# Optimization experiments

Hardware: AMD Instinct MI355X
Metric: run time of the kernel (lower is better)

## Reference

```python
import jax, jax.numpy as jnp
import numpy as np

L, B = 64, 7          # n_layers, n_bit_options
EPS = 0.02            # sinkhorn entropic regularizer
ITERS = 200           # sinkhorn iterations
TINY = 1e-40


def setup_inputs() -> dict:
    key = jax.random.key(0)
    k1, k2, k3, k4 = jax.random.split(key, 4)
    theta = jax.random.normal(k1, (L, B), dtype=jnp.float32)
    phi = jax.random.normal(k2, (B,), dtype=jnp.float32)
    # layer sizes (param counts), positive; matches layer_sizes buffer usage
    n = jax.random.uniform(k3, (L,), dtype=jnp.float32, minval=4096.0, maxval=262144.0)
    sens = jax.random.uniform(k4, (L,), dtype=jnp.float32)
    sens = sens / sens.sum()  # update_sensitivity normalizes to a distribution
    bits = jnp.arange(2, 2 + B, dtype=jnp.float32)
    err = 2.0 ** (-2.0 * bits)  # quantization error per bitwidth
    return {"theta": theta, "phi": phi, "n": n, "sens": sens, "err": err}


def reference(theta, phi, n, sens, err):
    # DiffAllocator.compute_P
    a = n / n.sum()                         # row marginal (buffer 'a')
    b = jax.nn.softmax(phi)                 # col marginal b()
    C = (n * sens)[:, None] * err[None, :]  # build_cost: [L,B]
    K = -(C - theta) / EPS                  # log-kernel
    log_a = jnp.log(a + TINY)
    log_b = jnp.log(b + TINY)
    f0 = jnp.zeros((L,), dtype=theta.dtype)
    g0 = jnp.zeros((B,), dtype=theta.dtype)

    def step(carry, _):
        f, g = carry
        f = log_a - jax.scipy.special.logsumexp(K + g[None, :], axis=1)
        g = log_b - jax.scipy.special.logsumexp(K + f[:, None], axis=0)
        return (f, g), None

    (f, g), _ = jax.lax.scan(step, (f0, g0), None, length=ITERS)
    P = jnp.exp(K + f[:, None] + g[None, :])
    return P / (P.sum() + TINY)
```

## Files before the change

kernel.cpp:

```cpp
#include <hip/hip_runtime.h>
#include <math.h>

#define NB 7
#define EPS_ 0.02f
#define ITERS_ 200
#define TINY_ 1e-40f
#define LOG2E_ 1.4426950408889634f
#define LN2_   0.6931471805599453f

__device__ __forceinline__ float exp2_hw(float x) {
#if __has_builtin(__builtin_amdgcn_exp2f)
    return __builtin_amdgcn_exp2f(x);
#else
    return __expf(x * LN2_);
#endif
}
__device__ __forceinline__ float log2_hw(float x) {
#if __has_builtin(__builtin_amdgcn_logf)
    return __builtin_amdgcn_logf(x);
#else
    return __logf(x) * LOG2E_;
#endif
}

template <int CTRL>
__device__ __forceinline__ float dpp_ident(float identity, float x) {
    return __int_as_float(__builtin_amdgcn_update_dpp(
        __float_as_int(identity), __float_as_int(x), CTRL, 0xF, 0xF, false));
}
__device__ __forceinline__ float readlane63(float x) {
    return __int_as_float(__builtin_amdgcn_readlane(__float_as_int(x), 63));
}
__device__ __forceinline__ float wave_sum_bcast(float s) {
    s += dpp_ident<0x111>(0.f, s);
    s += dpp_ident<0x112>(0.f, s);
    s += dpp_ident<0x114>(0.f, s);
    s += dpp_ident<0x118>(0.f, s);
    s += dpp_ident<0x142>(0.f, s);
    s += dpp_ident<0x143>(0.f, s);
    return readlane63(s);
}
__device__ __forceinline__ float wave_max_bcast(float m) {
    const float NI = __int_as_float(0xff800000);
    m = fmaxf(m, dpp_ident<0x111>(NI, m));
    m = fmaxf(m, dpp_ident<0x112>(NI, m));
    m = fmaxf(m, dpp_ident<0x114>(NI, m));
    m = fmaxf(m, dpp_ident<0x118>(NI, m));
    m = fmaxf(m, dpp_ident<0x142>(NI, m));
    m = fmaxf(m, dpp_ident<0x143>(NI, m));
    return readlane63(m);
}

#define WAVE_MAX7(v0,v1,v2,v3,v4,v5,v6, m0,m1,m2,m3,m4,m5,m6)                 \
  {                                                                           \
    float r0,r1,r2,r3,r4,r5,r6;                                               \
    asm("v_mov_b32 %0, %14\n\t"                                               \
        "v_mov_b32 %1, %15\n\t"                                               \
        "v_mov_b32 %2, %16\n\t"                                               \
        "v_mov_b32 %3, %17\n\t"                                               \
        "v_mov_b32 %4, %18\n\t"                                               \
        "v_mov_b32 %5, %19\n\t"                                               \
        "v_mov_b32 %6, %20\n\t"                                               \
        "v_max_f32_dpp %0, %0, %0 row_shr:1 row_mask:0xf bank_mask:0xf\n\t"   \
        "v_max_f32_dpp %1, %1, %1 row_shr:1 row_mask:0xf bank_mask:0xf\n\t"   \
        "v_max_f32_dpp %2, %2, %2 row_shr:1 row_mask:0xf bank_mask:0xf\n\t"   \
        "v_max_f32_dpp %3, %3, %3 row_shr:1 row_mask:0xf bank_mask:0xf\n\t"   \
        "v_max_f32_dpp %4, %4, %4 row_shr:1 row_mask:0xf bank_mask:0xf\n\t"   \
        "v_max_f32_dpp %5, %5, %5 row_shr:1 row_mask:0xf bank_mask:0xf\n\t"   \
        "v_max_f32_dpp %6, %6, %6 row_shr:1 row_mask:0xf bank_mask:0xf\n\t"   \
        "v_max_f32_dpp %0, %0, %0 row_shr:2 row_mask:0xf bank_mask:0xf\n\t"   \
        "v_max_f32_dpp %1, %1, %1 row_shr:2 row_mask:0xf bank_mask:0xf\n\t"   \
        "v_max_f32_dpp %2, %2, %2 row_shr:2 row_mask:0xf bank_mask:0xf\n\t"   \
        "v_max_f32_dpp %3, %3, %3 row_shr:2 row_mask:0xf bank_mask:0xf\n\t"   \
        "v_max_f32_dpp %4, %4, %4 row_shr:2 row_mask:0xf bank_mask:0xf\n\t"   \
        "v_max_f32_dpp %5, %5, %5 row_shr:2 row_mask:0xf bank_mask:0xf\n\t"   \
        "v_max_f32_dpp %6, %6, %6 row_shr:2 row_mask:0xf bank_mask:0xf\n\t"   \
        "v_max_f32_dpp %0, %0, %0 row_shr:4 row_mask:0xf bank_mask:0xf\n\t"   \
        "v_max_f32_dpp %1, %1, %1 row_shr:4 row_mask:0xf bank_mask:0xf\n\t"   \
        "v_max_f32_dpp %2, %2, %2 row_shr:4 row_mask:0xf bank_mask:0xf\n\t"   \
        "v_max_f32_dpp %3, %3, %3 row_shr:4 row_mask:0xf bank_mask:0xf\n\t"   \
        "v_max_f32_dpp %4, %4, %4 row_shr:4 row_mask:0xf bank_mask:0xf\n\t"   \
        "v_max_f32_dpp %5, %5, %5 row_shr:4 row_mask:0xf bank_mask:0xf\n\t"   \
        "v_max_f32_dpp %6, %6, %6 row_shr:4 row_mask:0xf bank_mask:0xf\n\t"   \
        "v_max_f32_dpp %0, %0, %0 row_shr:8 row_mask:0xf bank_mask:0xf\n\t"   \
        "v_max_f32_dpp %1, %1, %1 row_shr:8 row_mask:0xf bank_mask:0xf\n\t"   \
        "v_max_f32_dpp %2, %2, %2 row_shr:8 row_mask:0xf bank_mask:0xf\n\t"   \
        "v_max_f32_dpp %3, %3, %3 row_shr:8 row_mask:0xf bank_mask:0xf\n\t"   \
        "v_max_f32_dpp %4, %4, %4 row_shr:8 row_mask:0xf bank_mask:0xf\n\t"   \
        "v_max_f32_dpp %5, %5, %5 row_shr:8 row_mask:0xf bank_mask:0xf\n\t"   \
        "v_max_f32_dpp %6, %6, %6 row_shr:8 row_mask:0xf bank_mask:0xf\n\t"   \
        "v_max_f32_dpp %0, %0, %0 row_bcast:15 row_mask:0xa bank_mask:0xf\n\t"\
        "v_max_f32_dpp %1, %1, %1 row_bcast:15 row_mask:0xa bank_mask:0xf\n\t"\
        "v_max_f32_dpp %2, %2, %2 row_bcast:15 row_mask:0xa bank_mask:0xf\n\t"\
        "v_max_f32_dpp %3, %3, %3 row_bcast:15 row_mask:0xa bank_mask:0xf\n\t"\
        "v_max_f32_dpp %4, %4, %4 row_bcast:15 row_mask:0xa bank_mask:0xf\n\t"\
        "v_max_f32_dpp %5, %5, %5 row_bcast:15 row_mask:0xa bank_mask:0xf\n\t"\
        "v_max_f32_dpp %6, %6, %6 row_bcast:15 row_mask:0xa bank_mask:0xf\n\t"\
        "v_max_f32_dpp %0, %0, %0 row_bcast:31 row_mask:0xc bank_mask:0xf\n\t"\
        "v_max_f32_dpp %1, %1, %1 row_bcast:31 row_mask:0xc bank_mask:0xf\n\t"\
        "v_max_f32_dpp %2, %2, %2 row_bcast:31 row_mask:0xc bank_mask:0xf\n\t"\
        "v_max_f32_dpp %3, %3, %3 row_bcast:31 row_mask:0xc bank_mask:0xf\n\t"\
        "v_max_f32_dpp %4, %4, %4 row_bcast:31 row_mask:0xc bank_mask:0xf\n\t"\
        "v_max_f32_dpp %5, %5, %5 row_bcast:31 row_mask:0xc bank_mask:0xf\n\t"\
        "v_max_f32_dpp %6, %6, %6 row_bcast:31 row_mask:0xc bank_mask:0xf\n\t"\
        "v_readlane_b32 %7, %0, 63\n\t"                                       \
        "v_readlane_b32 %8, %1, 63\n\t"                                       \
        "v_readlane_b32 %9, %2, 63\n\t"                                       \
        "v_readlane_b32 %10, %3, 63\n\t"                                      \
        "v_readlane_b32 %11, %4, 63\n\t"                                      \
        "v_readlane_b32 %12, %5, 63\n\t"                                      \
        "v_readlane_b32 %13, %6, 63\n\t"                                      \
        "s_nop 1"                                                             \
        : "=&v"(r0), "=&v"(r1), "=&v"(r2), "=&v"(r3),                         \
          "=&v"(r4), "=&v"(r5), "=&v"(r6),                                    \
          "=s"(m0), "=s"(m1), "=s"(m2), "=s"(m3),                             \
          "=s"(m4), "=s"(m5), "=s"(m6)                                        \
        : "v"(v0), "v"(v1), "v"(v2), "v"(v3), "v"(v4), "v"(v5), "v"(v6));     \
  }

#define WAVE_SUM7(e0,e1,e2,e3,e4,e5,e6, s0_,s1_,s2_,s3_,s4_,s5_,s6_)          \
    asm("s_nop 1\n\t"                                                         \
        "v_add_f32_dpp %0, %0, %0 row_shr:1 row_mask:0xf bank_mask:0xf\n\t"   \
        "v_add_f32_dpp %1, %1, %1 row_shr:1 row_mask:0xf bank_mask:0xf\n\t"   \
        "v_add_f32_dpp %2, %2, %2 row_shr:1 row_mask:0xf bank_mask:0xf\n\t"   \
        "v_add_f32_dpp %3, %3, %3 row_shr:1 row_mask:0xf bank_mask:0xf\n\t"   \
        "v_add_f32_dpp %4, %4, %4 row_shr:1 row_mask:0xf bank_mask:0xf\n\t"   \
        "v_add_f32_dpp %5, %5, %5 row_shr:1 row_mask:0xf bank_mask:0xf\n\t"   \
        "v_add_f32_dpp %6, %6, %6 row_shr:1 row_mask:0xf bank_mask:0xf\n\t"   \
        "v_add_f32_dpp %0, %0, %0 row_shr:2 row_mask:0xf bank_mask:0xf\n\t"   \
        "v_add_f32_dpp %1, %1, %1 row_shr:2 row_mask:0xf bank_mask:0xf\n\t"   \
        "v_add_f32_dpp %2, %2, %2 row_shr:2 row_mask:0xf bank_mask:0xf\n\t"   \
        "v_add_f32_dpp %3, %3, %3 row_shr:2 row_mask:0xf bank_mask:0xf\n\t"   \
        "v_add_f32_dpp %4, %4, %4 row_shr:2 row_mask:0xf bank_mask:0xf\n\t"   \
        "v_add_f32_dpp %5, %5, %5 row_shr:2 row_mask:0xf bank_mask:0xf\n\t"   \
        "v_add_f32_dpp %6, %6, %6 row_shr:2 row_mask:0xf bank_mask:0xf\n\t"   \
        "v_add_f32_dpp %0, %0, %0 row_shr:4 row_mask:0xf bank_mask:0xf\n\t"   \
        "v_add_f32_dpp %1, %1, %1 row_shr:4 row_mask:0xf bank_mask:0xf\n\t"   \
        "v_add_f32_dpp %2, %2, %2 row_shr:4 row_mask:0xf bank_mask:0xf\n\t"   \
        "v_add_f32_dpp %3, %3, %3 row_shr:4 row_mask:0xf bank_mask:0xf\n\t"   \
        "v_add_f32_dpp %4, %4, %4 row_shr:4 row_mask:0xf bank_mask:0xf\n\t"   \
        "v_add_f32_dpp %5, %5, %5 row_shr:4 row_mask:0xf bank_mask:0xf\n\t"   \
        "v_add_f32_dpp %6, %6, %6 row_shr:4 row_mask:0xf bank_mask:0xf\n\t"   \
        "v_add_f32_dpp %0, %0, %0 row_shr:8 row_mask:0xf bank_mask:0xf\n\t"   \
        "v_add_f32_dpp %1, %1, %1 row_shr:8 row_mask:0xf bank_mask:0xf\n\t"   \
        "v_add_f32_dpp %2, %2, %2 row_shr:8 row_mask:0xf bank_mask:0xf\n\t"   \
        "v_add_f32_dpp %3, %3, %3 row_shr:8 row_mask:0xf bank_mask:0xf\n\t"   \
        "v_add_f32_dpp %4, %4, %4 row_shr:8 row_mask:0xf bank_mask:0xf\n\t"   \
        "v_add_f32_dpp %5, %5, %5 row_shr:8 row_mask:0xf bank_mask:0xf\n\t"   \
        "v_add_f32_dpp %6, %6, %6 row_shr:8 row_mask:0xf bank_mask:0xf\n\t"   \
        "v_add_f32_dpp %0, %0, %0 row_bcast:15 row_mask:0xa bank_mask:0xf\n\t"\
        "v_add_f32_dpp %1, %1, %1 row_bcast:15 row_mask:0xa bank_mask:0xf\n\t"\
        "v_add_f32_dpp %2, %2, %2 row_bcast:15 row_mask:0xa bank_mask:0xf\n\t"\
        "v_add_f32_dpp %3, %3, %3 row_bcast:15 row_mask:0xa bank_mask:0xf\n\t"\
        "v_add_f32_dpp %4, %4, %4 row_bcast:15 row_mask:0xa bank_mask:0xf\n\t"\
        "v_add_f32_dpp %5, %5, %5 row_bcast:15 row_mask:0xa bank_mask:0xf\n\t"\
        "v_add_f32_dpp %6, %6, %6 row_bcast:15 row_mask:0xa bank_mask:0xf\n\t"\
        "v_add_f32_dpp %0, %0, %0 row_bcast:31 row_mask:0xc bank_mask:0xf\n\t"\
        "v_add_f32_dpp %1, %1, %1 row_bcast:31 row_mask:0xc bank_mask:0xf\n\t"\
        "v_add_f32_dpp %2, %2, %2 row_bcast:31 row_mask:0xc bank_mask:0xf\n\t"\
        "v_add_f32_dpp %3, %3, %3 row_bcast:31 row_mask:0xc bank_mask:0xf\n\t"\
        "v_add_f32_dpp %4, %4, %4 row_bcast:31 row_mask:0xc bank_mask:0xf\n\t"\
        "v_add_f32_dpp %5, %5, %5 row_bcast:31 row_mask:0xc bank_mask:0xf\n\t"\
        "v_add_f32_dpp %6, %6, %6 row_bcast:31 row_mask:0xc bank_mask:0xf\n\t"\
        "v_readlane_b32 %7, %0, 63\n\t"                                       \
        "v_readlane_b32 %8, %1, 63\n\t"                                       \
        "v_readlane_b32 %9, %2, 63\n\t"                                       \
        "v_readlane_b32 %10, %3, 63\n\t"                                      \
        "v_readlane_b32 %11, %4, 63\n\t"                                      \
        "v_readlane_b32 %12, %5, 63\n\t"                                      \
        "v_readlane_b32 %13, %6, 63\n\t"                                      \
        "s_nop 1"                                                             \
        : "+v"(e0), "+v"(e1), "+v"(e2), "+v"(e3),                             \
          "+v"(e4), "+v"(e5), "+v"(e6),                                       \
          "=s"(s0_), "=s"(s1_), "=s"(s2_), "=s"(s3_),                         \
          "=s"(s4_), "=s"(s5_), "=s"(s6_))

__global__ __launch_bounds__(64) void sinkhorn_kernel(
    const float* __restrict__ theta,
    const float* __restrict__ phi,
    const float* __restrict__ n,
    const float* __restrict__ sens,
    const float* __restrict__ err,
    float* __restrict__ out)
{
    const int lane = threadIdx.x;

    const float ni = n[lane];
    const float si = sens[lane];

    const float kscale = LOG2E_ / EPS_;
    float K2[NB];
    #pragma unroll
    for (int j = 0; j < NB; ++j)
        K2[j] = (theta[lane * NB + j] - ni * si * err[j]) * kscale;

    const float nsum   = wave_sum_bcast(ni);
    const float log_a2 = log2_hw(ni / nsum + TINY_);

    float t2v[NB];
    #pragma unroll
    for (int j = 0; j < NB; ++j) t2v[j] = phi[j] * LOG2E_;
    float pmax = t2v[0];
    #pragma unroll
    for (int j = 1; j < NB; ++j) pmax = fmaxf(pmax, t2v[j]);
    float psum = 0.f;
    #pragma unroll
    for (int j = 0; j < NB; ++j) psum += exp2_hw(t2v[j] - pmax);
    const float lps = log2_hw(psum);
    float log_b2[NB], cb[NB];
    #pragma unroll
    for (int j = 0; j < NB; ++j) {
        log_b2[j] = log2_hw(exp2_hw(t2v[j] - pmax - lps) + TINY_);
        cb[j]     = log_b2[j] - log_a2;
    }

    float t[NB];
    #pragma unroll
    for (int j = 0; j < NB; ++j) t[j] = K2[j] - log_b2[j];

    const float LOF = __int_as_float(0x0D800000);
    const float HIF = __int_as_float(0x71800000);
    const unsigned LO = 0x0D800000u, HI = 0x71800000u;

    for (int it = 0; it < ITERS_; ++it) {
        float a0 = t[0] + cb[0], a1 = t[1] + cb[1], a2 = t[2] + cb[2],
              a3 = t[3] + cb[3], a4 = t[4] + cb[4], a5 = t[5] + cb[5],
              a6 = t[6] + cb[6];
        float s = ((exp2_hw(a0) + exp2_hw(a1)) + (exp2_hw(a2) + exp2_hw(a3)))
                + ((exp2_hw(a4) + exp2_hw(a5)) + exp2_hw(a6));
        float L;
        const bool ok = (s >= LOF) && (s <= HIF);
        if (__ballot(ok) == ~0ull) {
            L = log2_hw(s);
        } else {
            float m = fmaxf(fmaxf(fmaxf(a0, a1), fmaxf(a2, a3)),
                            fmaxf(fmaxf(a4, a5), a6));
            float s2 = ((exp2_hw(a0 - m) + exp2_hw(a1 - m))
                      + (exp2_hw(a2 - m) + exp2_hw(a3 - m)))
                     + ((exp2_hw(a4 - m) + exp2_hw(a5 - m)) + exp2_hw(a6 - m));
            L = m + log2_hw(s2);
        }

        float q0 = t[0] - L, q1 = t[1] - L, q2 = t[2] - L, q3 = t[3] - L,
              q4 = t[4] - L, q5 = t[5] - L, q6 = t[6] - L;
        float e0 = exp2_hw(q0), e1 = exp2_hw(q1), e2 = exp2_hw(q2),
              e3 = exp2_hw(q3), e4 = exp2_hw(q4), e5 = exp2_hw(q5),
              e6 = exp2_hw(q6);
        float ss0, ss1, ss2, ss3, ss4, ss5, ss6;
        WAVE_SUM7(e0, e1, e2, e3, e4, e5, e6, ss0, ss1, ss2, ss3, ss4, ss5, ss6);

        const unsigned u0 = __float_as_uint(ss0), u1 = __float_as_uint(ss1),
                       u2 = __float_as_uint(ss2), u3 = __float_as_uint(ss3),
                       u4 = __float_as_uint(ss4), u5 = __float_as_uint(ss5),
                       u6 = __float_as_uint(ss6);
        const unsigned umin = min(min(min(u0, u1), min(u2, u3)),
                                  min(min(u4, u5), u6));
        const unsigned umax = max(max(max(u0, u1), max(u2, u3)),
                                  max(max(u4, u5), u6));
        if (umin < LO || umax > HI) {
            float M0, M1, M2, M3, M4, M5, M6;
            WAVE_MAX7(q0, q1, q2, q3, q4, q5, q6, M0, M1, M2, M3, M4, M5, M6);
            e0 = exp2_hw(q0 - M0); e1 = exp2_hw(q1 - M1);
            e2 = exp2_hw(q2 - M2); e3 = exp2_hw(q3 - M3);
            e4 = exp2_hw(q4 - M4); e5 = exp2_hw(q5 - M5);
            e6 = exp2_hw(q6 - M6);
            WAVE_SUM7(e0, e1, e2, e3, e4, e5, e6, ss0, ss1, ss2, ss3, ss4, ss5, ss6);
            t[0] = q0 - (M0 + log2_hw(ss0)); t[1] = q1 - (M1 + log2_hw(ss1));
            t[2] = q2 - (M2 + log2_hw(ss2)); t[3] = q3 - (M3 + log2_hw(ss3));
            t[4] = q4 - (M4 + log2_hw(ss4)); t[5] = q5 - (M5 + log2_hw(ss5));
            t[6] = q6 - (M6 + log2_hw(ss6));
        } else {
            t[0] = q0 - log2_hw(ss0); t[1] = q1 - log2_hw(ss1);
            t[2] = q2 - log2_hw(ss2); t[3] = q3 - log2_hw(ss3);
            t[4] = q4 - log2_hw(ss4); t[5] = q5 - log2_hw(ss5);
            t[6] = q6 - log2_hw(ss6);
        }
    }

    const float NI = __int_as_float(0xff800000);
    float x[NB];
    float m = NI;
    #pragma unroll
    for (int j = 0; j < NB; ++j) {
        x[j] = t[j] + log_b2[j];
        m = fmaxf(m, x[j]);
    }
    m = wave_max_bcast(m);

    float p[NB];
    float s = 0.f;
    #pragma unroll
    for (int j = 0; j < NB; ++j) {
        p[j] = exp2_hw(x[j] - m);
        s += p[j];
    }
    s = wave_sum_bcast(s);

    const float inv = 1.0f / (s + exp2_hw(-132.87712379549449f - m));
    #pragma unroll
    for (int j = 0; j < NB; ++j)
        out[lane * NB + j] = p[j] * inv;
}

extern "C" void kernel_launch(void* const* d_in, const int* in_sizes, int n_in,
                              void* d_out, int out_size, void* d_ws, size_t ws_size,
                              hipStream_t stream) {
    const float* theta = (const float*)d_in[0];
    const float* phi   = (const float*)d_in[1];
    const float* n     = (const float*)d_in[2];
    const float* sens  = (const float*)d_in[3];
    const float* err   = (const float*)d_in[4];
    float* out = (float*)d_out;

    sinkhorn_kernel<<<1, 64, 0, stream>>>(theta, phi, n, sens, err, out);
}
```

Baseline: 123.2 us.

## Switch last Sinkhorn iterations from log-domain to scaled linear-domain updates

Splits the 200 Sinkhorn iterations into 120 log-domain iterations followed by 80 linear-domain iterations. The linear phase works on exponentiated scalings with multiplies and hardware reciprocals instead of exp2/log2 and wave max reductions. The final normalization then uses the linear-domain values directly. The intent is to cut transcendental and reduction work per iteration. The risk is underflow or overflow in the linear domain, guarded only by a clamp on the column sums, and it assumes the first phase has converged enough for the linear phase to be stable on these inputs.

```diff
diff --git a/kernel.cpp b/kernel.cpp
--- a/kernel.cpp
+++ b/kernel.cpp
@@ -3,7 +3,8 @@
 
 #define NB 7
 #define EPS_ 0.02f
-#define ITERS_ 200
+#define ITERS1_ 120
+#define ITERS2_ 80
 #define TINY_ 1e-40f
 #define LOG2E_ 1.4426950408889634f
 #define LN2_   0.6931471805599453f
@@ -20,6 +21,13 @@
     return __builtin_amdgcn_logf(x);
 #else
     return __logf(x) * LOG2E_;
+#endif
+}
+__device__ __forceinline__ float rcp_hw(float x) {
+#if __has_builtin(__builtin_amdgcn_rcpf)
+    return __builtin_amdgcn_rcpf(x);
+#else
+    return 1.0f / x;
 #endif
 }
 
@@ -195,7 +203,8 @@
         K2[j] = (theta[lane * NB + j] - ni * si * err[j]) * kscale;
 
     const float nsum   = wave_sum_bcast(ni);
-    const float log_a2 = log2_hw(ni / nsum + TINY_);
+    const float aT     = ni / nsum + TINY_;
+    const float log_a2 = log2_hw(aT);
 
     float t2v[NB];
     #pragma unroll
@@ -207,10 +216,11 @@
     #pragma unroll
     for (int j = 0; j < NB; ++j) psum += exp2_hw(t2v[j] - pmax);
     const float lps = log2_hw(psum);
-    float log_b2[NB], cb[NB];
+    float bT[NB], log_b2[NB], cb[NB];
     #pragma unroll
     for (int j = 0; j < NB; ++j) {
-        log_b2[j] = log2_hw(exp2_hw(t2v[j] - pmax - lps) + TINY_);
+        bT[j]     = exp2_hw(t2v[j] - pmax - lps) + TINY_;
+        log_b2[j] = log2_hw(bT[j]);
         cb[j]     = log_b2[j] - log_a2;
     }
 
@@ -222,7 +232,7 @@
     const float HIF = __int_as_float(0x71800000);
     const unsigned LO = 0x0D800000u, HI = 0x71800000u;
 
-    for (int it = 0; it < ITERS_; ++it) {
+    for (int it = 0; it < ITERS1_; ++it) {
         float a0 = t[0] + cb[0], a1 = t[1] + cb[1], a2 = t[2] + cb[2],
               a3 = t[3] + cb[3], a4 = t[4] + cb[4], a5 = t[5] + cb[5],
               a6 = t[6] + cb[6];
@@ -277,29 +287,52 @@
         }
     }
 
-    const float NI = __int_as_float(0xff800000);
-    float x[NB];
-    float m = NI;
+    float U[NB], B[NB];
     #pragma unroll
     for (int j = 0; j < NB; ++j) {
-        x[j] = t[j] + log_b2[j];
-        m = fmaxf(m, x[j]);
-    }
-    m = wave_max_bcast(m);
-
-    float p[NB];
-    float s = 0.f;
+        U[j] = exp2_hw(t[j]);
+        B[j] = exp2_hw(cb[j]);
+    }
+
+    const float SSMIN = 1e-37f;
+
+    for (int it = 0; it < ITERS2_; ++it) {
+        float p0 = U[0] * B[0], p1 = U[1] * B[1], p2 = U[2] * B[2],
+              p3 = U[3] * B[3], p4 = U[4] * B[4], p5 = U[5] * B[5],
+              p6 = U[6] * B[6];
+        const float s = ((p0 + p1) + (p2 + p3)) + ((p4 + p5) + p6);
+        const float rs = rcp_hw(s);
+        float w0 = U[0] * rs, w1 = U[1] * rs, w2 = U[2] * rs,
+              w3 = U[3] * rs, w4 = U[4] * rs, w5 = U[5] * rs,
+              w6 = U[6] * rs;
+
+        float c0 = w0, c1 = w1, c2 = w2, c3 = w3, c4 = w4, c5 = w5, c6 = w6;
+        float ss0, ss1, ss2, ss3, ss4, ss5, ss6;
+        WAVE_SUM7(c0, c1, c2, c3, c4, c5, c6, ss0, ss1, ss2, ss3, ss4, ss5, ss6);
+
+        const float r0 = rcp_hw(fmaxf(ss0, SSMIN));
+        const float r1 = rcp_hw(fmaxf(ss1, SSMIN));
+        const float r2 = rcp_hw(fmaxf(ss2, SSMIN));
+        const float r3 = rcp_hw(fmaxf(ss3, SSMIN));
+        const float r4 = rcp_hw(fmaxf(ss4, SSMIN));
+        const float r5 = rcp_hw(fmaxf(ss5, SSMIN));
+        const float r6 = rcp_hw(fmaxf(ss6, SSMIN));
+        U[0] = w0 * r0; U[1] = w1 * r1; U[2] = w2 * r2; U[3] = w3 * r3;
+        U[4] = w4 * r4; U[5] = w5 * r5; U[6] = w6 * r6;
+    }
+
+    float pr[NB];
+    float rowsum = 0.f;
     #pragma unroll
     for (int j = 0; j < NB; ++j) {
-        p[j] = exp2_hw(x[j] - m);
-        s += p[j];
-    }
-    s = wave_sum_bcast(s);
-
-    const float inv = 1.0f / (s + exp2_hw(-132.87712379549449f - m));
+        pr[j] = U[j] * bT[j];
+        rowsum += pr[j];
+    }
+    const float total = wave_sum_bcast(rowsum);
+    const float inv = 1.0f / (total + TINY_);
     #pragma unroll
     for (int j = 0; j < NB; ++j)
-        out[lane * NB + j] = p[j] * inv;
+        out[lane * NB + j] = pr[j] * inv;
 }
 
 extern "C" void kernel_launch(void* const* d_in, const int* in_sizes, int n_in,
```

Measured after the change: 117.6 us. -4.6%, faster.
